# Performance work log

Hardware: AMD Instinct MI355X
Metric: run time of the kernel (lower is better)

The kernel has to match this reference:

```python
import jax, jax.numpy as jnp
import numpy as np

DMODEL = 1024
N_MAMBAS = 4
D_INNER = 2 * DMODEL          # expand = 2
D_STATE = 16                  # mamba_ssm default
D_CONV = 4                    # mamba_ssm default
DT_RANK = DMODEL // 16        # ceil(d_model/16) = 64


def setup_inputs() -> dict:
    key = jax.random.key(0)
    ks = jax.random.split(key, 8)
    B, L, n = 2, 4096, N_MAMBAS
    f32 = jnp.float32
    x = jax.random.normal(ks[0], (B, L, DMODEL), f32)
    in_w = jax.random.normal(ks[1], (n, 2 * D_INNER, DMODEL), f32) * 0.02
    conv_w = jax.random.normal(ks[2], (n, D_INNER, D_CONV), f32) * 0.1
    conv_b = jnp.zeros((n, D_INNER), f32)
    xproj_w = jax.random.normal(ks[3], (n, DT_RANK + 2 * D_STATE, D_INNER), f32) * 0.02
    dt_w = jax.random.normal(ks[4], (n, D_INNER, DT_RANK), f32) * 0.02
    # softplus-inverse of dt_init ~ 0.01 (mamba-style dt bias init)
    dt_b = jnp.log(jnp.expm1(jnp.full((n, D_INNER), 0.01, f32)))
    # S4D-real init: A_log = log(1..d_state)
    A_log = jnp.log(jnp.broadcast_to(jnp.arange(1, D_STATE + 1, dtype=f32), (n, D_INNER, D_STATE)))
    D_skip = jnp.ones((n, D_INNER), f32)
    out_w = jax.random.normal(ks[5], (n, DMODEL, D_INNER), f32) * 0.02
    return dict(x=x, in_w=in_w, conv_w=conv_w, conv_b=conv_b, xproj_w=xproj_w,
                dt_w=dt_w, dt_b=dt_b, A_log=A_log, D_skip=D_skip, out_w=out_w)


def _mamba(x, in_w, conv_w, conv_b, xproj_w, dt_w, dt_b, A_log, D_skip, out_w):
    # x: (B, Lc, D)
    Bb = x.shape[0]
    xz = jnp.einsum('bld,ed->ble', x, in_w)                 # (B, Lc, 2*D_INNER)
    xi, z = jnp.split(xz, 2, axis=-1)
    # causal depthwise conv over time
    xc = jnp.transpose(xi, (0, 2, 1))                       # (B, D_INNER, Lc)
    xc = jax.lax.conv_general_dilated(xc, conv_w[:, None, :], (1,),
                                      [(D_CONV - 1, 0)], feature_group_count=D_INNER)
    xi = jax.nn.silu(jnp.transpose(xc + conv_b[None, :, None], (0, 2, 1)))  # (B, Lc, D_INNER)
    proj = jnp.einsum('bld,ed->ble', xi, xproj_w)           # (B, Lc, DT_RANK + 2*D_STATE)
    dt = proj[..., :DT_RANK]
    Bm = proj[..., DT_RANK:DT_RANK + D_STATE]
    Cm = proj[..., DT_RANK + D_STATE:]
    dt = jax.nn.softplus(jnp.einsum('blr,dr->bld', dt, dt_w) + dt_b)  # (B, Lc, D_INNER)
    A = -jnp.exp(A_log)                                     # (D_INNER, D_STATE)

    def step(h, inp):
        dt_t, B_t, C_t, x_t = inp                           # (B,Di),(B,Ds),(B,Ds),(B,Di)
        dA = jnp.exp(dt_t[:, :, None] * A)                  # (B, Di, Ds)
        h = dA * h + dt_t[:, :, None] * B_t[:, None, :] * x_t[:, :, None]
        return h, jnp.einsum('bds,bs->bd', h, C_t)

    h0 = jnp.zeros((Bb, D_INNER, D_STATE), x.dtype)
    xs_t = (jnp.swapaxes(dt, 0, 1), jnp.swapaxes(Bm, 0, 1),
            jnp.swapaxes(Cm, 0, 1), jnp.swapaxes(xi, 0, 1))
    _, ys = jax.lax.scan(step, h0, xs_t)                    # (Lc, B, D_INNER)
    y = jnp.swapaxes(ys, 0, 1) + xi * D_skip                # (B, Lc, D_INNER)
    y = y * jax.nn.silu(z)
    return jnp.einsum('ble,de->bld', y, out_w)              # (B, Lc, D)


def reference(x, in_w, conv_w, conv_b, xproj_w, dt_w, dt_b, A_log, D_skip, out_w):
    B, L, D = x.shape
    n = N_MAMBAS
    # strided slices x[:, i::n] == reshape(B, L//n, n, D)[:, :, i]
    xs = jnp.transpose(x.reshape(B, L // n, n, D), (2, 0, 1, 3))   # (n, B, Lc, D)
    ys = jax.vmap(_mamba)(xs, in_w, conv_w, conv_b, xproj_w,
                          dt_w, dt_b, A_log, D_skip, out_w)        # (n, B, Lc, D)
    # torch.cat(dim=1) concatenates per-mamba outputs block-wise along seq
    return jnp.transpose(ys, (1, 0, 2, 3)).reshape(B, L, D)
```

## Files before the change

### kernel.cpp

```cpp
#include <hip/hip_runtime.h>
#include <math.h>

#define DM   1024
#define DI   2048
#define DSn  16
#define DTR  64
#define PW   96
#define LS   1024
#define NCH  16
#define CL   64
#define XKS  8

typedef unsigned short u16;
typedef unsigned int   u32;
typedef __attribute__((ext_vector_type(8))) short bf16x8;
typedef __attribute__((ext_vector_type(8))) unsigned short u16x8;
typedef __attribute__((ext_vector_type(4))) float f32x4;

__device__ __forceinline__ void bar_lds() {
  asm volatile("s_waitcnt lgkmcnt(0)\n\ts_barrier" ::: "memory");
}

__device__ __forceinline__ void split2(float f, u16& hi, u16& lo) {
  union { float f; unsigned int u; } v; v.f = f;
  hi = (u16)(v.u >> 16);
  union { unsigned int u; float f; } w; w.u = v.u & 0xffff0000u;
  union { float f; unsigned int u; } r; r.f = f - w.f;
  lo = (u16)(r.u >> 16);
}

template<int ROWS>
__device__ __forceinline__ bf16x8 frag(const u16* T, int l4, int row) {
  return *(const bf16x8*)&T[(l4 * ROWS + row) * 8];
}

template<int ROWS>
__device__ __forceinline__ void stage16f(const float* a, u16* Th, u16* Tl, int ra, int half) {
  #pragma unroll
  for (int q = 0; q < 2; ++q) {
    u16x8 vh, vl;
    #pragma unroll
    for (int c = 0; c < 8; ++c) {
      u16 h_, l_;
      split2(a[q * 8 + c], h_, l_);
      vh[c] = h_; vl[c] = l_;
    }
    const int slot = ((half * 2 + q) * ROWS + ra) * 8;
    *(u16x8*)&Th[slot] = vh;
    *(u16x8*)&Tl[slot] = vl;
  }
}

__global__ __launch_bounds__(256) void k_split_x(
    const float* __restrict__ x, u16* __restrict__ xh, u16* __restrict__ xl, int ib0)
{
  const int idx = blockIdx.x * 256 + threadIdx.x;
  const int t = idx >> 8, kq = (idx & 255) * 4;
  const int gt = ib0 * 1024 + t;
  const int j = gt & (LS - 1), ib = gt >> 10;
  const int i = ib >> 1, bb = ib & 1;
  const float4 v = *(const float4*)&x[(size_t)(bb * 4096 + j * 4 + i) * DM + kq];
  ushort4 vh, vl;
  split2(v.x, vh.x, vl.x); split2(v.y, vh.y, vl.y);
  split2(v.z, vh.z, vl.z); split2(v.w, vh.w, vl.w);
  *(ushort4*)&xh[(size_t)t * DM + kq] = vh;
  *(ushort4*)&xl[(size_t)t * DM + kq] = vl;
}

#define KGP 2064
__global__ __launch_bounds__(512, 2) void k_inproj(
    const u16* __restrict__ xh, const u16* __restrict__ xl,
    const float* __restrict__ inwf,
    float* __restrict__ xz, int ib0, int swz)
{
  __shared__ __align__(16) u16 L[2][4][4][KGP];
  const int tid = threadIdx.x;
  int mblk, nblk;
  if (swz) {
    const int o = blockIdx.x;
    const int xcd = o & 7, within = o >> 3;
    mblk = xcd * 4 + (within & 3);
    nblk = within >> 2;
  } else {
    mblk = blockIdx.x; nblk = blockIdx.y;
  }
  const int m0 = mblk << 8, n0 = nblk << 8;
  const int ib = ib0 + (m0 >> 10);
  const int il = (ib >> 1) - (ib0 >> 1);
  const int ra = tid >> 1, half = tid & 1;
  const u16* Aph = xh + (size_t)(m0 + ra) * DM + half * 16;
  const u16* Apl = xl + (size_t)(m0 + ra) * DM + half * 16;
  const float* Bpf = inwf + ((size_t)il * 4096 + n0 + ra) * DM + half * 16;
  const int w = tid >> 6, lane = tid & 63;
  const int wr = w >> 2, wc = w & 3;
  const int l15 = lane & 15, l4 = lane >> 4;

  f32x4 acc[8][4];
  #pragma unroll
  for (int a_ = 0; a_ < 8; ++a_)
    #pragma unroll
    for (int b_ = 0; b_ < 4; ++b_) acc[a_][b_] = (f32x4)(0.f);

  u16x8 ah2[2], al2[2];
  float br[16];

  auto LOADG = [&](int kt) {
    const int k0 = kt * 32;
    ah2[0] = *(const u16x8*)(Aph + k0);
    ah2[1] = *(const u16x8*)(Aph + k0 + 8);
    al2[0] = *(const u16x8*)(Apl + k0);
    al2[1] = *(const u16x8*)(Apl + k0 + 8);
    *(f32x4*)&br[0]  = *(const f32x4*)(Bpf + k0);
    *(f32x4*)&br[4]  = *(const f32x4*)(Bpf + k0 + 4);
    *(f32x4*)&br[8]  = *(const f32x4*)(Bpf + k0 + 8);
    *(f32x4*)&br[12] = *(const f32x4*)(Bpf + k0 + 12);
  };
  auto STORE = [&](int b) {
    #pragma unroll
    for (int q = 0; q < 2; ++q) {
      const int kg = half * 2 + q;
      *(u16x8*)&L[b][0][kg][ra * 8] = ah2[q];
      *(u16x8*)&L[b][1][kg][ra * 8] = al2[q];
      u16x8 vh, vl;
      #pragma unroll
      for (int c = 0; c < 8; ++c) {
        u16 h_, l_;
        split2(br[q * 8 + c], h_, l_);
        vh[c] = h_; vl[c] = l_;
      }
      *(u16x8*)&L[b][2][kg][ra * 8] = vh;
      *(u16x8*)&L[b][3][kg][ra * 8] = vl;
    }
  };
  auto COMPUTE = [&](int b) {
    bf16x8 bh[4], bl[4];
    #pragma unroll
    for (int nf = 0; nf < 4; ++nf) {
      const int col = wc * 64 + nf * 16 + l15;
      bh[nf] = *(const bf16x8*)&L[b][2][l4][col * 8];
      bl[nf] = *(const bf16x8*)&L[b][3][l4][col * 8];
    }
    #pragma unroll
    for (int mf = 0; mf < 8; ++mf) {
      const int row = wr * 128 + mf * 16 + l15;
      bf16x8 ah = *(const bf16x8*)&L[b][0][l4][row * 8];
      bf16x8 al = *(const bf16x8*)&L[b][1][l4][row * 8];
      #pragma unroll
      for (int nf = 0; nf < 4; ++nf) {
        acc[mf][nf] = __builtin_amdgcn_mfma_f32_16x16x32_bf16(ah, bh[nf], acc[mf][nf], 0, 0, 0);
        acc[mf][nf] = __builtin_amdgcn_mfma_f32_16x16x32_bf16(ah, bl[nf], acc[mf][nf], 0, 0, 0);
        acc[mf][nf] = __builtin_amdgcn_mfma_f32_16x16x32_bf16(al, bh[nf], acc[mf][nf], 0, 0, 0);
      }
    }
  };

  const int nk = DM / 32;
  LOADG(0);
  STORE(0);
  if (nk > 1) LOADG(1);
  bar_lds();
  for (int kt = 0; kt < nk; ++kt) {
    const int c = kt & 1;
    if (kt + 1 < nk) STORE(c ^ 1);
    if (kt + 2 < nk) LOADG(kt + 2);
    COMPUTE(c);
    bar_lds();
  }

  #pragma unroll
  for (int mf = 0; mf < 8; ++mf) {
    const int row = m0 + wr * 128 + mf * 16 + l4 * 4;
    #pragma unroll
    for (int nf = 0; nf < 4; ++nf) {
      const int col = n0 + wc * 64 + nf * 16 + l15;
      #pragma unroll
      for (int r = 0; r < 4; ++r)
        xz[(size_t)(row + r) * (2 * DI) + col] = acc[mf][nf][r];
    }
  }
}

__global__ __launch_bounds__(256) void k_conv(
    const float* __restrict__ xz, const float* __restrict__ convw,
    const float* __restrict__ convb, float* __restrict__ xib,
    int ib0, int ntok)
{
  const int idx = blockIdx.x * 256 + threadIdx.x;
  if (idx >= ntok * (DI / 4)) return;
  const int t = idx / (DI / 4);
  const int c = (idx - t * (DI / 4)) * 4;
  const int j = t & (LS - 1);
  const int i = (ib0 + (t >> 10)) >> 1;
  float4 acc = *(const float4*)&convb[(size_t)i * DI + c];
  float4 wt[4];
  #pragma unroll
  for (int q = 0; q < 4; ++q)
    wt[q] = *(const float4*)&convw[((size_t)i * DI + c + q) * 4];
  #pragma unroll
  for (int k = 0; k < 4; ++k) {
    const int j2 = j + k - 3;
    if (j2 >= 0) {
      const float4 v = *(const float4*)&xz[(size_t)(t + k - 3) * (2 * DI) + c];
      acc.x = fmaf(v.x, ((const float*)&wt[0])[k], acc.x);
      acc.y = fmaf(v.y, ((const float*)&wt[1])[k], acc.y);
      acc.z = fmaf(v.z, ((const float*)&wt[2])[k], acc.z);
      acc.w = fmaf(v.w, ((const float*)&wt[3])[k], acc.w);
    }
  }
  float4 o;
  o.x = acc.x / (1.f + __expf(-acc.x));
  o.y = acc.y / (1.f + __expf(-acc.y));
  o.z = acc.z / (1.f + __expf(-acc.z));
  o.w = acc.w / (1.f + __expf(-acc.w));
  *(float4*)&xib[(size_t)t * DI + c] = o;
}

__global__ __launch_bounds__(256) void k_xproj_part(
    const float* __restrict__ xif, const float* __restrict__ xwf,
    float* __restrict__ Pp, int ib0, int ntok)
{
  __shared__ __align__(16) u16 Ah[2][4*64*8], Al[2][4*64*8];
  __shared__ __align__(16) u16 Bh[2][4*96*8], Bl[2][4*96*8];
  const int tid = threadIdx.x;
  const int m0 = blockIdx.x << 6;
  const int ks = blockIdx.y;
  const int kbase = ks * (DI / XKS);
  const int ib = ib0 + (m0 >> 10);
  const int il = (ib >> 1) - (ib0 >> 1);
  const int ra = tid >> 1, half = tid & 1;
  const bool hasA = (tid < 128);
  const bool hasB = (tid < 192);
  const float* Apf = xif + (size_t)(m0 + ra) * DI + kbase + half * 16;
  const float* Bpf = xwf + ((size_t)il * PW + ra) * DI + kbase + half * 16;
  const int w = tid >> 6, lane = tid & 63;
  const int l15 = lane & 15, l4 = lane >> 4;

  f32x4 acc[6];
  #pragma unroll
  for (int b_ = 0; b_ < 6; ++b_) acc[b_] = (f32x4)(0.f);

  float ar[16], br[16];
  auto LOADAB = [&](int kt) {
    const int k0 = kt * 32;
    if (hasA) {
      #pragma unroll
      for (int q = 0; q < 4; ++q) *(f32x4*)&ar[q*4] = *(const f32x4*)(Apf + k0 + q*4);
    }
    if (hasB) {
      #pragma unroll
      for (int q = 0; q < 4; ++q) *(f32x4*)&br[q*4] = *(const f32x4*)(Bpf + k0 + q*4);
    }
  };
  auto STORE = [&](int b) {
    if (hasA) stage16f<64>(ar, Ah[b], Al[b], ra, half);
    if (hasB) stage16f<96>(br, Bh[b], Bl[b], ra, half);
  };
  auto COMPUTE = [&](int b) {
    const int arow = w * 16 + l15;
    bf16x8 ah = frag<64>(Ah[b], l4, arow);
    bf16x8 al = frag<64>(Al[b], l4, arow);
    #pragma unroll
    for (int nf = 0; nf < 6; ++nf) {
      const int col = nf * 16 + l15;
      bf16x8 bh = frag<96>(Bh[b], l4, col);
      bf16x8 bl = frag<96>(Bl[b], l4, col);
      acc[nf] = __builtin_amdgcn_mfma_f32_16x16x32_bf16(ah, bh, acc[nf], 0, 0, 0);
      acc[nf] = __builtin_amdgcn_mfma_f32_16x16x32_bf16(ah, bl, acc[nf], 0, 0, 0);
      acc[nf] = __builtin_amdgcn_mfma_f32_16x16x32_bf16(al, bh, acc[nf], 0, 0, 0);
    }
  };

  const int nk = (DI / XKS) / 32;
  LOADAB(0);
  STORE(0);
  LOADAB(1);
  bar_lds();
  for (int kt = 0; kt < nk; ++kt) {
    const int c = kt & 1;
    if (kt + 1 < nk) STORE(c ^ 1);
    if (kt + 2 < nk) LOADAB(kt + 2);
    COMPUTE(c);
    bar_lds();
  }

  float* outp = Pp + (size_t)ks * ntok * PW;
  const int row = m0 + w * 16 + l4 * 4;
  #pragma unroll
  for (int nf = 0; nf < 6; ++nf) {
    const int col = nf * 16 + l15;
    #pragma unroll
    for (int r = 0; r < 4; ++r)
      outp[(size_t)(row + r) * PW + col] = acc[nf][r];
  }
}

__global__ __launch_bounds__(256) void k_xproj_red(
    const float* __restrict__ Pp, float* __restrict__ projb, int ntok)
{
  const int idx = blockIdx.x * 256 + threadIdx.x;
  if (idx >= ntok * PW) return;
  const size_t plane = (size_t)ntok * PW;
  float s = 0.f;
  #pragma unroll
  for (int ks = 0; ks < XKS; ++ks) s += Pp[(size_t)ks * plane + idx];
  projb[idx] = s;
}

__global__ __launch_bounds__(256) void k_dtproj(
    const float* __restrict__ proj, const float* __restrict__ dtw,
    const float* __restrict__ dtbias, float* __restrict__ dtout,
    int dstride, int ib0)
{
  __shared__ float As[16][132];
  __shared__ float Bs[16][132];
  const int tid = threadIdx.x;
  const int n0 = blockIdx.x << 7;
  const int m0 = blockIdx.y << 7;
  const int ib = ib0 + (m0 >> 10);
  const int i  = ib >> 1;
  const int ar = tid >> 2, kq = tid & 3;
  const float* A0 = proj + (size_t)(m0 + ar) * PW + kq * 4;
  const float* A1 = A0 + (size_t)64 * PW;
  const float* Wb = dtw + (size_t)i * DI * DTR;
  const float* B0 = Wb + (size_t)(n0 + ar) * DTR + kq * 4;
  const float* B1 = B0 + (size_t)64 * DTR;
  const int tx = tid & 15, ty = tid >> 4;
  float acc[8][8] = {};
  for (int kt = 0; kt < DTR / 16; ++kt) {
    const int k0 = kt * 16;
    float4 a0 = *(const float4*)(A0 + k0);
    float4 a1 = *(const float4*)(A1 + k0);
    float4 b0 = *(const float4*)(B0 + k0);
    float4 b1 = *(const float4*)(B1 + k0);
    __syncthreads();
    As[kq*4+0][ar] = a0.x; As[kq*4+1][ar] = a0.y; As[kq*4+2][ar] = a0.z; As[kq*4+3][ar] = a0.w;
    As[kq*4+0][ar+64] = a1.x; As[kq*4+1][ar+64] = a1.y; As[kq*4+2][ar+64] = a1.z; As[kq*4+3][ar+64] = a1.w;
    Bs[kq*4+0][ar] = b0.x; Bs[kq*4+1][ar] = b0.y; Bs[kq*4+2][ar] = b0.z; Bs[kq*4+3][ar] = b0.w;
    Bs[kq*4+0][ar+64] = b1.x; Bs[kq*4+1][ar+64] = b1.y; Bs[kq*4+2][ar+64] = b1.z; Bs[kq*4+3][ar+64] = b1.w;
    __syncthreads();
    #pragma unroll
    for (int k = 0; k < 16; ++k) {
      const float4 av0 = *(const float4*)&As[k][ty*8];
      const float4 av1 = *(const float4*)&As[k][ty*8+4];
      const float4 bv0 = *(const float4*)&Bs[k][tx*8];
      const float4 bv1 = *(const float4*)&Bs[k][tx*8+4];
      const float aa[8] = {av0.x,av0.y,av0.z,av0.w,av1.x,av1.y,av1.z,av1.w};
      const float bv[8] = {bv0.x,bv0.y,bv0.z,bv0.w,bv1.x,bv1.y,bv1.z,bv1.w};
      #pragma unroll
      for (int r = 0; r < 8; ++r)
        #pragma unroll
        for (int c = 0; c < 8; ++c)
          acc[r][c] = fmaf(aa[r], bv[c], acc[r][c]);
    }
  }
  float bias[8];
  #pragma unroll
  for (int c = 0; c < 8; ++c) bias[c] = dtbias[(size_t)i * DI + n0 + tx*8 + c];
  #pragma unroll
  for (int r = 0; r < 8; ++r) {
    const int t = m0 + ty*8 + r;
    #pragma unroll
    for (int c = 0; c < 8; ++c) {
      float u = acc[r][c] + bias[c];
      float sp = (u > 20.f) ? u : log1pf(__expf(u));
      dtout[(size_t)t * dstride + n0 + tx*8 + c] = sp;
    }
  }
}

__global__ __launch_bounds__(256) void k_scan_part(
    const float* __restrict__ projb, const float* dtp, int dstride,
    const float* __restrict__ xib, const float* __restrict__ A_log,
    float* __restrict__ Pbuf, float* __restrict__ Hbuf, int ib0)
{
  const int d = blockIdx.x * 256 + threadIdx.x;
  const int ch = blockIdx.y, lib = blockIdx.z;
  const int i = (ib0 + lib) >> 1;
  const size_t gd = (size_t)i * DI + d;
  __shared__ float bs[CL][DSn];
  const size_t trow = (size_t)lib * LS + (size_t)ch * CL;
  for (int p = threadIdx.x; p < CL * DSn; p += 256) {
    const int jj = p >> 4, ss = p & 15;
    bs[jj][ss] = projb[(trow + jj) * PW + DTR + ss];
  }
  float A[DSn], P[DSn], h[DSn];
  #pragma unroll
  for (int s = 0; s < DSn; ++s) {
    A[s] = -__expf(A_log[gd * DSn + s]);
    P[s] = 1.f; h[s] = 0.f;
  }
  __syncthreads();
  float dt_c = dtp[trow * dstride + d];
  float xi_c = xib[trow * DI + d];
  for (int j = 0; j < CL; ++j) {
    float dt_n = 0.f, xi_n = 0.f;
    if (j + 1 < CL) {
      dt_n = dtp[(trow + j + 1) * dstride + d];
      xi_n = xib[(trow + j + 1) * DI + d];
    }
    const float dx = dt_c * xi_c;
    #pragma unroll
    for (int s = 0; s < DSn; ++s) {
      const float dA = __expf(dt_c * A[s]);
      P[s] *= dA;
      h[s] = fmaf(dA, h[s], dx * bs[j][s]);
    }
    dt_c = dt_n; xi_c = xi_n;
  }
  const size_t base = ((size_t)(lib * NCH + ch) * DSn) * DI + d;
  #pragma unroll
  for (int s = 0; s < DSn; ++s) {
    Pbuf[base + (size_t)s * DI] = P[s];
    Hbuf[base + (size_t)s * DI] = h[s];
  }
}

__global__ __launch_bounds__(256) void k_scan_mid(
    float* __restrict__ Pbuf, const float* __restrict__ Hbuf, int nib)
{
  const int idx = blockIdx.x * 256 + threadIdx.x;
  if (idx >= nib * DSn * DI) return;
  const int d = idx & (DI - 1);
  const int s = (idx >> 11) & 15;
  const int lib = idx >> 15;
  const size_t stride = (size_t)DSn * DI;
  const size_t base = ((size_t)lib * NCH * DSn + s) * DI + d;
  float carry = 0.f;
  for (int c = 0; c < NCH; ++c) {
    const size_t o = base + (size_t)c * stride;
    const float p = Pbuf[o];
    const float hl = Hbuf[o];
    Pbuf[o] = carry;
    carry = fmaf(p, carry, hl);
  }
}

__global__ __launch_bounds__(256) void k_scan_full(
    const float* __restrict__ projb, const float* dtp, int dstride,
    float* xibio, const float* xzz,
    const float* __restrict__ A_log, const float* __restrict__ D_skip,
    const float* __restrict__ Pbuf, int ib0)
{
  const int d = blockIdx.x * 256 + threadIdx.x;
  const int ch = blockIdx.y, lib = blockIdx.z;
  const int i = (ib0 + lib) >> 1;
  const size_t gd = (size_t)i * DI + d;
  __shared__ float bs[CL][2 * DSn];
  const size_t trow = (size_t)lib * LS + (size_t)ch * CL;
  for (int p = threadIdx.x; p < CL * 2 * DSn; p += 256) {
    const int jj = p >> 5, ss = p & 31;
    bs[jj][ss] = projb[(trow + jj) * PW + DTR + ss];
  }
  float A[DSn], h[DSn];
  const size_t hbase = ((size_t)(lib * NCH + ch) * DSn) * DI + d;
  #pragma unroll
  for (int s = 0; s < DSn; ++s) {
    A[s] = -__expf(A_log[gd * DSn + s]);
    h[s] = Pbuf[hbase + (size_t)s * DI];
  }
  const float Dsk = D_skip[gd];
  __syncthreads();
  float dt_c = dtp[trow * dstride + d];
  float xi_c = xibio[trow * DI + d];
  float z_c  = xzz[trow * (2 * DI) + DI + d];
  for (int j = 0; j < CL; ++j) {
    float dt_n = 0.f, xi_n = 0.f, z_n = 0.f;
    if (j + 1 < CL) {
      dt_n = dtp[(trow + j + 1) * dstride + d];
      xi_n = xibio[(trow + j + 1) * DI + d];
      z_n  = xzz[(trow + j + 1) * (2 * DI) + DI + d];
    }
    const float dx = dt_c * xi_c;
    float y = 0.f;
    #pragma unroll
    for (int s = 0; s < DSn; ++s) {
      const float dA = __expf(dt_c * A[s]);
      h[s] = fmaf(dA, h[s], dx * bs[j][s]);
      y = fmaf(h[s], bs[j][DSn + s], y);
    }
    const float sz = z_c / (1.f + __expf(-z_c));
    const float val = (y + xi_c * Dsk) * sz;
    u16 vh, vl;
    split2(val, vh, vl);
    ((u32*)xibio)[(trow + j) * DI + d] = ((u32)vh << 16) | (u32)vl;
    dt_c = dt_n; xi_c = xi_n; z_c = z_n;
  }
}

__global__ __launch_bounds__(256) void k_outproj(
    const u32* __restrict__ ybp, const float* __restrict__ owf,
    float* __restrict__ out, int ib0)
{
  __shared__ __align__(16) u16 Ah[2][4*128*8], Al[2][4*128*8];
  __shared__ __align__(16) u16 Bh[2][4*128*8], Bl[2][4*128*8];
  const int tid = threadIdx.x;
  const int m0 = blockIdx.x << 7;
  const int n0 = blockIdx.y << 7;
  const int ib = ib0 + (m0 >> 10);
  const int i = ib >> 1, bb = ib & 1;
  const int il = i - (ib0 >> 1);
  const int ra = tid >> 1, half = tid & 1;
  const u32* Ap = ybp + (size_t)(m0 + ra) * DI + half * 16;
  const int rb = tid >> 1;
  const float* Bpf = owf + ((size_t)il * DM + n0 + rb) * DI + half * 16;
  const int w = tid >> 6, lane = tid & 63;
  const int wr = w >> 1, wc = w & 1;
  const int l15 = lane & 15, l4 = lane >> 4;

  f32x4 acc[4][4];
  #pragma unroll
  for (int a_ = 0; a_ < 4; ++a_)
    #pragma unroll
    for (int b_ = 0; b_ < 4; ++b_) acc[a_][b_] = (f32x4)(0.f);

  uint4 qa[4];
  float br[16];
  auto LOADG = [&](int kt) {
    const int k0 = kt * 32;
    qa[0] = *(const uint4*)(Ap + k0);     qa[1] = *(const uint4*)(Ap + k0 + 4);
    qa[2] = *(const uint4*)(Ap + k0 + 8); qa[3] = *(const uint4*)(Ap + k0 + 12);
    #pragma unroll
    for (int q = 0; q < 4; ++q) *(f32x4*)&br[q*4] = *(const f32x4*)(Bpf + k0 + q*4);
  };
  auto STORE = [&](int b) {
    #pragma unroll
    for (int g = 0; g < 2; ++g) {
      const u32 e[8] = { qa[2*g].x, qa[2*g].y, qa[2*g].z, qa[2*g].w,
                         qa[2*g+1].x, qa[2*g+1].y, qa[2*g+1].z, qa[2*g+1].w };
      u16x8 vh, vl;
      #pragma unroll
      for (int c = 0; c < 8; ++c) { vh[c] = (u16)(e[c] >> 16); vl[c] = (u16)(e[c] & 0xffffu); }
      const int slot = ((half*2+g)*128 + ra)*8;
      *(u16x8*)&Ah[b][slot] = vh;
      *(u16x8*)&Al[b][slot] = vl;
    }
    stage16f<128>(br, Bh[b], Bl[b], rb, half);
  };
  auto COMPUTE = [&](int b) {
    bf16x8 ah[4], al[4];
    #pragma unroll
    for (int mf = 0; mf < 4; ++mf) {
      const int row = wr * 64 + mf * 16 + l15;
      ah[mf] = frag<128>(Ah[b], l4, row);
      al[mf] = frag<128>(Al[b], l4, row);
    }
    #pragma unroll
    for (int nf = 0; nf < 4; ++nf) {
      const int col = wc * 64 + nf * 16 + l15;
      bf16x8 bh = frag<128>(Bh[b], l4, col);
      bf16x8 bl = frag<128>(Bl[b], l4, col);
      #pragma unroll
      for (int mf = 0; mf < 4; ++mf) {
        acc[mf][nf] = __builtin_amdgcn_mfma_f32_16x16x32_bf16(ah[mf], bh, acc[mf][nf], 0, 0, 0);
        acc[mf][nf] = __builtin_amdgcn_mfma_f32_16x16x32_bf16(ah[mf], bl, acc[mf][nf], 0, 0, 0);
        acc[mf][nf] = __builtin_amdgcn_mfma_f32_16x16x32_bf16(al[mf], bh, acc[mf][nf], 0, 0, 0);
      }
    }
  };

  const int nk = DI / 32;
  LOADG(0);
  STORE(0);
  LOADG(1);
  bar_lds();
  for (int kt = 0; kt < nk; ++kt) {
    const int c = kt & 1;
    if (kt + 1 < nk) STORE(c ^ 1);
    if (kt + 2 < nk) LOADG(kt + 2);
    COMPUTE(c);
    bar_lds();
  }

  #pragma unroll
  for (int mf = 0; mf < 4; ++mf) {
    const int t0 = m0 + wr * 64 + mf * 16 + l4 * 4;
    #pragma unroll
    for (int nf = 0; nf < 4; ++nf) {
      const int col = n0 + wc * 64 + nf * 16 + l15;
      #pragma unroll
      for (int r = 0; r < 4; ++r) {
        const int j = (t0 + r) & (LS - 1);
        out[(size_t)(bb * 4096 + i * 1024 + j) * DM + col] = acc[mf][nf][r];
      }
    }
  }
}

extern "C" void kernel_launch(void* const* d_in, const int* in_sizes, int n_in,
                              void* d_out, int out_size, void* d_ws, size_t ws_size,
                              hipStream_t stream) {
  (void)in_sizes; (void)n_in; (void)out_size;
  const float* x       = (const float*)d_in[0];
  const float* in_w    = (const float*)d_in[1];
  const float* conv_w  = (const float*)d_in[2];
  const float* conv_b  = (const float*)d_in[3];
  const float* xproj_w = (const float*)d_in[4];
  const float* dt_w    = (const float*)d_in[5];
  const float* dt_b    = (const float*)d_in[6];
  const float* A_log   = (const float*)d_in[7];
  const float* D_skip  = (const float*)d_in[8];
  const float* out_w   = (const float*)d_in[9];
  float* out = (float*)d_out;
  const dim3 blk(256);

  const size_t needSP = ((size_t)8192 * 4096 + (size_t)8192 * 2048 + (size_t)8192 * 96) * 4;
  if (ws_size >= needSP) {
    const size_t nt = 8192;
    float* xz    = (float*)d_ws;
    float* xib   = xz + nt * (2 * DI);
    float* projb = xib + nt * DI;
    u16* xph  = (u16*)d_out;  u16* xpl  = xph + nt * DM;
    float* Pp = (float*)d_out;
    float* Pbuf = (float*)d_out;
    float* Hbuf = Pbuf + (size_t)8 * NCH * DSn * DI;
    float* dtz = xz;
    u32* ybp  = (u32*)xib;

    k_split_x<<<dim3((int)nt), blk, 0, stream>>>(x, xph, xpl, 0);
    k_inproj<<<dim3(512), dim3(512), 0, stream>>>(xph, xpl, in_w, xz, 0, 1);
    k_conv<<<dim3((int)(nt*(DI/4)/256)), blk, 0, stream>>>(xz, conv_w, conv_b, xib, 0, (int)nt);
    k_xproj_part<<<dim3((int)(nt/64), XKS), blk, 0, stream>>>(xib, xproj_w, Pp, 0, (int)nt);
    k_xproj_red<<<dim3((int)(nt*PW/256)), blk, 0, stream>>>(Pp, projb, (int)nt);
    k_dtproj<<<dim3(DI/128, (int)(nt/128)), blk, 0, stream>>>(projb, dt_w, dt_b, dtz, 2*DI, 0);
    k_scan_part<<<dim3(DI/256, NCH, 8), blk, 0, stream>>>(projb, dtz, 2*DI, xib, A_log, Pbuf, Hbuf, 0);
    k_scan_mid<<<dim3(8 * DSn * DI / 256), blk, 0, stream>>>(Pbuf, Hbuf, 8);
    k_scan_full<<<dim3(DI/256, NCH, 8), blk, 0, stream>>>(projb, dtz, 2*DI, xib, xz, A_log, D_skip, Pbuf, 0);
    k_outproj<<<dim3((int)(nt/128), 8), blk, 0, stream>>>(ybp, out_w, out, 0);
    return;
  }

  auto needFB = [](int nib) -> size_t { return (size_t)nib * 29753344ull; };
  const int step = (ws_size >= needFB(4)) ? 4 : 2;

  for (int ib0 = 0; ib0 < 8; ib0 += step) {
    const int nib = step;
    const size_t nt = (size_t)nib * LS;
    const int i0 = ib0 >> 1;
    float* xz    = (float*)d_ws;
    float* xib   = xz + nt * (2 * DI);
    float* projb = xib + nt * DI;
    float* SH    = projb + nt * PW;
    u16* xph  = (u16*)SH;  u16* xpl = xph + nt * DM;
    float* Pp = SH;
    float* Pbuf = SH;
    float* Hbuf = Pbuf + (size_t)nib * NCH * DSn * DI / 2;
    float* dtz = xz;
    u32* ybp  = (u32*)xib;

    k_split_x<<<dim3((int)nt), blk, 0, stream>>>(x, xph, xpl, ib0);
    k_inproj<<<dim3((int)(nt/256), 16), dim3(512), 0, stream>>>(xph, xpl, in_w + (size_t)i0*4096*DM, xz, ib0, 0);
    k_conv<<<dim3((int)(nt*(DI/4)/256)), blk, 0, stream>>>(xz, conv_w, conv_b, xib, ib0, (int)nt);
    k_xproj_part<<<dim3((int)(nt/64), XKS), blk, 0, stream>>>(xib, xproj_w + (size_t)i0*PW*DI, Pp, ib0, (int)nt);
    k_xproj_red<<<dim3((int)(nt*PW/256)), blk, 0, stream>>>(Pp, projb, (int)nt);
    k_dtproj<<<dim3(DI/128, (int)(nt/128)), blk, 0, stream>>>(projb, dt_w, dt_b, dtz, 2*DI, ib0);
    k_scan_part<<<dim3(DI/256, NCH, nib), blk, 0, stream>>>(projb, dtz, 2*DI, xib, A_log, Pbuf, Hbuf, ib0);
    k_scan_mid<<<dim3(nib * DSn * DI / 256), blk, 0, stream>>>(Pbuf, Hbuf, nib);
    k_scan_full<<<dim3(DI/256, NCH, nib), blk, 0, stream>>>(projb, dtz, 2*DI, xib, xz, A_log, D_skip, Pbuf, ib0);
    k_outproj<<<dim3((int)(nt/128), 8), blk, 0, stream>>>(ybp, out_w + (size_t)i0*DM*DI, out, ib0);
  }
}
```

Measured before the change: 626.3 us.

## Load A operand tiles directly into LDS via global_load_lds in in-proj GEMM

Replaces the register round-trip for the pre-split bf16 A operand (xh/xl) in the input-projection GEMM with direct global-to-LDS loads, with vmcnt-based barriers to overlap these with the fp32 B loads and their split. This frees VGPRs and drops the ds_write instructions for A. The change also lowers XKS from 8 to 4, which alters the split-K factor of a later kernel. The vmcnt(4) accounting is fragile and depends on exact instruction ordering.

```diff
diff --git a/kernel.cpp b/kernel.cpp
--- a/kernel.cpp
+++ b/kernel.cpp
@@ -9,7 +9,7 @@
 #define LS   1024
 #define NCH  16
 #define CL   64
-#define XKS  8
+#define XKS  4
 
 typedef unsigned short u16;
 typedef unsigned int   u32;
@@ -17,8 +17,18 @@
 typedef __attribute__((ext_vector_type(8))) unsigned short u16x8;
 typedef __attribute__((ext_vector_type(4))) float f32x4;
 
+#define GLOAD16(gp, lp) \
+  __builtin_amdgcn_global_load_lds((const __attribute__((address_space(1))) void*)(gp), \
+                                   (__attribute__((address_space(3))) void*)(lp), 16, 0, 0)
+
 __device__ __forceinline__ void bar_lds() {
   asm volatile("s_waitcnt lgkmcnt(0)\n\ts_barrier" ::: "memory");
+}
+__device__ __forceinline__ void bar_v4() {
+  asm volatile("s_waitcnt vmcnt(4) lgkmcnt(0)\n\ts_barrier" ::: "memory");
+}
+__device__ __forceinline__ void bar_v0() {
+  asm volatile("s_waitcnt vmcnt(0) lgkmcnt(0)\n\ts_barrier" ::: "memory");
 }
 
 __device__ __forceinline__ void split2(float f, u16& hi, u16& lo) {
@@ -88,39 +98,39 @@
   const int ib = ib0 + (m0 >> 10);
   const int il = (ib >> 1) - (ib0 >> 1);
   const int ra = tid >> 1, half = tid & 1;
-  const u16* Aph = xh + (size_t)(m0 + ra) * DM + half * 16;
-  const u16* Apl = xl + (size_t)(m0 + ra) * DM + half * 16;
   const float* Bpf = inwf + ((size_t)il * 4096 + n0 + ra) * DM + half * 16;
   const int w = tid >> 6, lane = tid & 63;
   const int wr = w >> 2, wc = w & 3;
   const int l15 = lane & 15, l4 = lane >> 4;
 
+  const int pA = w >> 2, kgA = w & 3;
+  const u16* agp = (pA ? xl : xh) + (size_t)(m0 + lane) * DM + kgA * 8;
+
   f32x4 acc[8][4];
   #pragma unroll
   for (int a_ = 0; a_ < 8; ++a_)
     #pragma unroll
     for (int b_ = 0; b_ < 4; ++b_) acc[a_][b_] = (f32x4)(0.f);
 
-  u16x8 ah2[2], al2[2];
   float br[16];
 
-  auto LOADG = [&](int kt) {
+  auto LOADB = [&](int kt) {
     const int k0 = kt * 32;
-    ah2[0] = *(const u16x8*)(Aph + k0);
-    ah2[1] = *(const u16x8*)(Aph + k0 + 8);
-    al2[0] = *(const u16x8*)(Apl + k0);
-    al2[1] = *(const u16x8*)(Apl + k0 + 8);
     *(f32x4*)&br[0]  = *(const f32x4*)(Bpf + k0);
     *(f32x4*)&br[4]  = *(const f32x4*)(Bpf + k0 + 4);
     *(f32x4*)&br[8]  = *(const f32x4*)(Bpf + k0 + 8);
     *(f32x4*)&br[12] = *(const f32x4*)(Bpf + k0 + 12);
   };
-  auto STORE = [&](int b) {
+  auto DMAA = [&](int b, int kt) {
+    const int k0 = kt * 32;
+    #pragma unroll
+    for (int q = 0; q < 4; ++q)
+      GLOAD16(agp + (size_t)(q * 64) * DM + k0, &L[b][pA][kgA][q * 64 * 8]);
+  };
+  auto STOREB = [&](int b) {
     #pragma unroll
     for (int q = 0; q < 2; ++q) {
       const int kg = half * 2 + q;
-      *(u16x8*)&L[b][0][kg][ra * 8] = ah2[q];
-      *(u16x8*)&L[b][1][kg][ra * 8] = al2[q];
       u16x8 vh, vl;
       #pragma unroll
       for (int c = 0; c < 8; ++c) {
@@ -155,16 +165,20 @@
   };
 
   const int nk = DM / 32;
-  LOADG(0);
-  STORE(0);
-  if (nk > 1) LOADG(1);
-  bar_lds();
+  LOADB(0);
+  DMAA(0, 0);
+  __builtin_amdgcn_sched_barrier(0);
+  STOREB(0);
+  LOADB(1);
+  bar_v4();
   for (int kt = 0; kt < nk; ++kt) {
     const int c = kt & 1;
-    if (kt + 1 < nk) STORE(c ^ 1);
-    if (kt + 2 < nk) LOADG(kt + 2);
+    if (kt + 1 < nk) DMAA(c ^ 1, kt + 1);
+    __builtin_amdgcn_sched_barrier(0);
+    if (kt + 1 < nk) STOREB(c ^ 1);
+    if (kt + 2 < nk) LOADB(kt + 2);
     COMPUTE(c);
-    bar_lds();
+    if (kt + 2 < nk) bar_v4(); else bar_v0();
   }
 
   #pragma unroll
```

Result: slower. 668.5 us (+6.7%).

## Use split-bf16 MFMA for dt projection GEMM and halve xproj K-split

Applied to the files above, without the earlier changes.

Rewrites the dt-projection GEMM (K=64) to split fp32 operands into high and low bf16 parts in LDS and accumulate three bf16 MFMA products, replacing the scalar FMA tiled loop. This moves the work onto the matrix cores while keeping near-fp32 accuracy. It also halves the xproj K-split factor, which means fewer partial planes to write and reduce but less parallelism in that GEMM.

```diff
diff --git a/kernel.cpp b/kernel.cpp
--- a/kernel.cpp
+++ b/kernel.cpp
@@ -9,7 +9,7 @@
 #define LS   1024
 #define NCH  16
 #define CL   64
-#define XKS  8
+#define XKS  4
 
 typedef unsigned short u16;
 typedef unsigned int   u32;
@@ -311,59 +311,84 @@
     const float* __restrict__ dtbias, float* __restrict__ dtout,
     int dstride, int ib0)
 {
-  __shared__ float As[16][132];
-  __shared__ float Bs[16][132];
+  __shared__ __align__(16) u16 Ah[8*128*8], Al[8*128*8];
+  __shared__ __align__(16) u16 Bh[8*128*8], Bl[8*128*8];
   const int tid = threadIdx.x;
   const int n0 = blockIdx.x << 7;
   const int m0 = blockIdx.y << 7;
   const int ib = ib0 + (m0 >> 10);
   const int i  = ib >> 1;
-  const int ar = tid >> 2, kq = tid & 3;
-  const float* A0 = proj + (size_t)(m0 + ar) * PW + kq * 4;
-  const float* A1 = A0 + (size_t)64 * PW;
-  const float* Wb = dtw + (size_t)i * DI * DTR;
-  const float* B0 = Wb + (size_t)(n0 + ar) * DTR + kq * 4;
-  const float* B1 = B0 + (size_t)64 * DTR;
-  const int tx = tid & 15, ty = tid >> 4;
-  float acc[8][8] = {};
-  for (int kt = 0; kt < DTR / 16; ++kt) {
-    const int k0 = kt * 16;
-    float4 a0 = *(const float4*)(A0 + k0);
-    float4 a1 = *(const float4*)(A1 + k0);
-    float4 b0 = *(const float4*)(B0 + k0);
-    float4 b1 = *(const float4*)(B1 + k0);
-    __syncthreads();
-    As[kq*4+0][ar] = a0.x; As[kq*4+1][ar] = a0.y; As[kq*4+2][ar] = a0.z; As[kq*4+3][ar] = a0.w;
-    As[kq*4+0][ar+64] = a1.x; As[kq*4+1][ar+64] = a1.y; As[kq*4+2][ar+64] = a1.z; As[kq*4+3][ar+64] = a1.w;
-    Bs[kq*4+0][ar] = b0.x; Bs[kq*4+1][ar] = b0.y; Bs[kq*4+2][ar] = b0.z; Bs[kq*4+3][ar] = b0.w;
-    Bs[kq*4+0][ar+64] = b1.x; Bs[kq*4+1][ar+64] = b1.y; Bs[kq*4+2][ar+64] = b1.z; Bs[kq*4+3][ar+64] = b1.w;
-    __syncthreads();
-    #pragma unroll
-    for (int k = 0; k < 16; ++k) {
-      const float4 av0 = *(const float4*)&As[k][ty*8];
-      const float4 av1 = *(const float4*)&As[k][ty*8+4];
-      const float4 bv0 = *(const float4*)&Bs[k][tx*8];
-      const float4 bv1 = *(const float4*)&Bs[k][tx*8+4];
-      const float aa[8] = {av0.x,av0.y,av0.z,av0.w,av1.x,av1.y,av1.z,av1.w};
-      const float bv[8] = {bv0.x,bv0.y,bv0.z,bv0.w,bv1.x,bv1.y,bv1.z,bv1.w};
-      #pragma unroll
-      for (int r = 0; r < 8; ++r)
-        #pragma unroll
-        for (int c = 0; c < 8; ++c)
-          acc[r][c] = fmaf(aa[r], bv[c], acc[r][c]);
-    }
-  }
-  float bias[8];
-  #pragma unroll
-  for (int c = 0; c < 8; ++c) bias[c] = dtbias[(size_t)i * DI + n0 + tx*8 + c];
-  #pragma unroll
-  for (int r = 0; r < 8; ++r) {
-    const int t = m0 + ty*8 + r;
-    #pragma unroll
-    for (int c = 0; c < 8; ++c) {
-      float u = acc[r][c] + bias[c];
-      float sp = (u > 20.f) ? u : log1pf(__expf(u));
-      dtout[(size_t)t * dstride + n0 + tx*8 + c] = sp;
+  const int ra = tid >> 1, half = tid & 1;
+  const float* Ap = proj + (size_t)(m0 + ra) * PW + half * 32;
+  const float* Bp = dtw + ((size_t)i * DI + n0 + ra) * DTR + half * 32;
+  const int w = tid >> 6, lane = tid & 63;
+  const int wr = w >> 1, wc = w & 1;
+  const int l15 = lane & 15, l4 = lane >> 4;
+
+  {
+    float av[32], bv[32];
+    #pragma unroll
+    for (int q = 0; q < 8; ++q) *(f32x4*)&av[q*4] = *(const f32x4*)(Ap + q*4);
+    #pragma unroll
+    for (int q = 0; q < 8; ++q) *(f32x4*)&bv[q*4] = *(const f32x4*)(Bp + q*4);
+    #pragma unroll
+    for (int q = 0; q < 4; ++q) {
+      u16x8 vh, vl, wh, wl;
+      #pragma unroll
+      for (int c = 0; c < 8; ++c) {
+        u16 h_, l_;
+        split2(av[q*8+c], h_, l_); vh[c] = h_; vl[c] = l_;
+        split2(bv[q*8+c], h_, l_); wh[c] = h_; wl[c] = l_;
+      }
+      const int slot = ((half*4 + q) * 128 + ra) * 8;
+      *(u16x8*)&Ah[slot] = vh; *(u16x8*)&Al[slot] = vl;
+      *(u16x8*)&Bh[slot] = wh; *(u16x8*)&Bl[slot] = wl;
+    }
+  }
+  __syncthreads();
+
+  f32x4 acc[4][4];
+  #pragma unroll
+  for (int a_ = 0; a_ < 4; ++a_)
+    #pragma unroll
+    for (int b_ = 0; b_ < 4; ++b_) acc[a_][b_] = (f32x4)(0.f);
+
+  #pragma unroll
+  for (int c = 0; c < 2; ++c) {
+    bf16x8 bh[4], bl[4];
+    #pragma unroll
+    for (int nf = 0; nf < 4; ++nf) {
+      const int col = wc * 64 + nf * 16 + l15;
+      bh[nf] = *(const bf16x8*)&Bh[((4*c + l4) * 128 + col) * 8];
+      bl[nf] = *(const bf16x8*)&Bl[((4*c + l4) * 128 + col) * 8];
+    }
+    #pragma unroll
+    for (int mf = 0; mf < 4; ++mf) {
+      const int row = wr * 64 + mf * 16 + l15;
+      bf16x8 ah = *(const bf16x8*)&Ah[((4*c + l4) * 128 + row) * 8];
+      bf16x8 al = *(const bf16x8*)&Al[((4*c + l4) * 128 + row) * 8];
+      #pragma unroll
+      for (int nf = 0; nf < 4; ++nf) {
+        acc[mf][nf] = __builtin_amdgcn_mfma_f32_16x16x32_bf16(ah, bh[nf], acc[mf][nf], 0, 0, 0);
+        acc[mf][nf] = __builtin_amdgcn_mfma_f32_16x16x32_bf16(ah, bl[nf], acc[mf][nf], 0, 0, 0);
+        acc[mf][nf] = __builtin_amdgcn_mfma_f32_16x16x32_bf16(al, bh[nf], acc[mf][nf], 0, 0, 0);
+      }
+    }
+  }
+
+  #pragma unroll
+  for (int nf = 0; nf < 4; ++nf) {
+    const int col = n0 + wc * 64 + nf * 16 + l15;
+    const float bias = dtbias[(size_t)i * DI + col];
+    #pragma unroll
+    for (int mf = 0; mf < 4; ++mf) {
+      const int t0 = m0 + wr * 64 + mf * 16 + l4 * 4;
+      #pragma unroll
+      for (int r = 0; r < 4; ++r) {
+        const float u = acc[mf][nf][r] + bias;
+        const float sp = (u > 20.f) ? u : log1pf(__expf(u));
+        dtout[(size_t)(t0 + r) * dstride + col] = sp;
+      }
     }
   }
 }
```

Result: faster. 604.7 us (-3.4%).
